# Kernel tuning notes

Hardware: AMD Instinct MI355X
Metric: run time of the kernel (lower is better)

The kernel has to match this reference:

```python
import jax, jax.numpy as jnp
import numpy as np

N_NODES = 100000
N_EDGES = 1600000
IN_F = 128
HID = 16
NEG_SLOPE = 0.2


def setup_inputs() -> dict:
    key = jax.random.key(0)
    ks = jax.random.split(key, 12)
    x = jax.random.normal(ks[0], (N_NODES, IN_F), dtype=jnp.float32)
    edge_index = jax.random.randint(ks[1], (2, N_EDGES), 0, N_NODES, dtype=jnp.int32)
    s1 = 1.0 / np.sqrt(IN_F)
    s2 = 1.0 / np.sqrt(2 * HID)
    # layer 1: heads=2, out=16, concat -> 32
    W1 = jax.random.normal(ks[2], (IN_F, 2 * HID), dtype=jnp.float32) * s1
    a_src1 = jax.random.normal(ks[3], (2, HID), dtype=jnp.float32) * s2
    a_dst1 = jax.random.normal(ks[4], (2, HID), dtype=jnp.float32) * s2
    b1 = jnp.zeros((2 * HID,), dtype=jnp.float32)
    # layer 2: heads=1, out=1
    W2 = jax.random.normal(ks[5], (2 * HID, 1), dtype=jnp.float32) * s2
    a_src2 = jax.random.normal(ks[6], (1, 1), dtype=jnp.float32)
    a_dst2 = jax.random.normal(ks[7], (1, 1), dtype=jnp.float32)
    b2 = jnp.zeros((1,), dtype=jnp.float32)
    return {"x": x, "edge_index": edge_index, "W1": W1, "a_src1": a_src1,
            "a_dst1": a_dst1, "b1": b1, "W2": W2, "a_src2": a_src2,
            "a_dst2": a_dst2, "b2": b2}


def gat_conv(x, src, dst, W, a_src, a_dst, bias, heads, out_ch, concat):
    # PyG GATConv: linear proj, per-edge leaky-relu score, segment softmax over
    # incoming edges (dst), scatter-add aggregation. Self loops already in src/dst.
    n = x.shape[0]
    h = (x @ W).reshape(n, heads, out_ch)                      # [N,H,C]
    alpha_s = (h * a_src[None]).sum(-1)                        # [N,H]
    alpha_d = (h * a_dst[None]).sum(-1)                        # [N,H]
    e = jax.nn.leaky_relu(alpha_s[src] + alpha_d[dst], NEG_SLOPE)  # [E,H]
    m = jax.lax.stop_gradient(jax.ops.segment_max(e, dst, num_segments=n))
    ex = jnp.exp(e - m[dst])
    denom = jax.ops.segment_sum(ex, dst, num_segments=n)       # [N,H]
    alpha = ex / (denom[dst] + 1e-16)                          # [E,H]
    out = jax.ops.segment_sum(alpha[..., None] * h[src], dst, num_segments=n)  # [N,H,C]
    out = out.reshape(n, heads * out_ch) if concat else out.mean(axis=1)
    return out + bias


def reference(x, edge_index, W1, a_src1, a_dst1, b1, W2, a_src2, a_dst2, b2):
    n = x.shape[0]
    loop = jnp.arange(n, dtype=edge_index.dtype)
    src = jnp.concatenate([edge_index[0], loop])
    dst = jnp.concatenate([edge_index[1], loop])
    h = jax.nn.elu(gat_conv(x, src, dst, W1, a_src1, a_dst1, b1, 2, HID, True))
    out = gat_conv(h, src, dst, W2, a_src2, a_dst2, b2, 1, 1, False)
    return out
```

## Files before the change

### kernel.cpp

```cpp
#include <hip/hip_runtime.h>
#include <math.h>

#define IN_F 128
#define C1 32
#define NEG 0.2f
#define BSZ 128
#define CAP 2560
#define EPB 16384
#define TPW 2

typedef _Float16 h16;
typedef _Float16 h16x2 __attribute__((ext_vector_type(2)));
typedef _Float16 h16x4 __attribute__((ext_vector_type(4)));
typedef _Float16 h16x8 __attribute__((ext_vector_type(8)));
typedef float f32x4 __attribute__((ext_vector_type(4)));

__device__ __forceinline__ float leaky(float x) { return x >= 0.f ? x : NEG * x; }

__global__ __launch_bounds__(256)
void k_fat(const float* __restrict__ x, const float* __restrict__ W1,
           const float* __restrict__ a_s, const float* __restrict__ a_d,
           h16* __restrict__ h1h, float* __restrict__ as1,
           float* __restrict__ ad1, int N,
           const int* __restrict__ ei, int E, int ET, int nbk,
           int* __restrict__ bcnt, int* __restrict__ ebuf, int nproj) {
    __shared__ int smem[2048];
    int t = threadIdx.x;
    if ((int)blockIdx.x < nproj) {
        int wid = t >> 6, lane = t & 63;
        int q = lane >> 4, r = lane & 15;
        h16x8 Bf[2][4];
        #pragma unroll
        for (int ct = 0; ct < 2; ++ct)
            #pragma unroll
            for (int kc = 0; kc < 4; ++kc)
                #pragma unroll
                for (int j = 0; j < 8; ++j)
                    Bf[ct][kc][j] = (h16)W1[(kc * 32 + q * 8 + j) * C1 + ct * 16 + r];
        float a_s0 = a_s[r], a_s1v = a_s[16 + r];
        float a_d0 = a_d[r], a_d1v = a_d[16 + r];
        #pragma unroll
        for (int tt = 0; tt < TPW; ++tt) {
            int tile = (blockIdx.x * 4 + wid) * TPW + tt;
            int m0 = tile << 4;
            if (m0 >= N) break;
            int row = m0 + r; if (row >= N) row = N - 1;
            const float* xr = x + (size_t)row * IN_F + q * 8;
            f32x4 acc0 = {0.f, 0.f, 0.f, 0.f};
            f32x4 acc1 = {0.f, 0.f, 0.f, 0.f};
            #pragma unroll
            for (int kc = 0; kc < 4; ++kc) {
                float4 xa = *(const float4*)(xr + kc * 32);
                float4 xb = *(const float4*)(xr + kc * 32 + 4);
                h16x8 A;
                A[0] = (h16)xa.x; A[1] = (h16)xa.y; A[2] = (h16)xa.z; A[3] = (h16)xa.w;
                A[4] = (h16)xb.x; A[5] = (h16)xb.y; A[6] = (h16)xb.z; A[7] = (h16)xb.w;
                acc0 = __builtin_amdgcn_mfma_f32_16x16x32_f16(A, Bf[0][kc], acc0, 0, 0, 0);
                acc1 = __builtin_amdgcn_mfma_f32_16x16x32_f16(A, Bf[1][kc], acc1, 0, 0, 0);
            }
            #pragma unroll
            for (int reg = 0; reg < 4; ++reg) {
                int node = m0 + q * 4 + reg;
                bool vld = node < N;
                float h0 = acc0[reg], h1 = acc1[reg];
                if (vld) {
                    h1h[(size_t)node * C1 + r]      = (h16)h0;
                    h1h[(size_t)node * C1 + 16 + r] = (h16)h1;
                }
                float s0 = h0 * a_s0, s1 = h1 * a_s1v;
                float d0 = h0 * a_d0, d1 = h1 * a_d1v;
                s0 += __shfl_xor(s0, 1); s0 += __shfl_xor(s0, 2); s0 += __shfl_xor(s0, 4); s0 += __shfl_xor(s0, 8);
                s1 += __shfl_xor(s1, 1); s1 += __shfl_xor(s1, 2); s1 += __shfl_xor(s1, 4); s1 += __shfl_xor(s1, 8);
                d0 += __shfl_xor(d0, 1); d0 += __shfl_xor(d0, 2); d0 += __shfl_xor(d0, 4); d0 += __shfl_xor(d0, 8);
                d1 += __shfl_xor(d1, 1); d1 += __shfl_xor(d1, 2); d1 += __shfl_xor(d1, 4); d1 += __shfl_xor(d1, 8);
                if (vld && r == 0) {
                    *(float2*)&as1[node * 2] = make_float2(s0, s1);
                    *(float2*)&ad1[node * 2] = make_float2(d0, d1);
                }
            }
        }
    } else {
        int* hist = smem;
        int* lcur = smem + 1024;
        int bid = blockIdx.x - nproj;
        hist[t] = 0; hist[t + 256] = 0; hist[t + 512] = 0; hist[t + 768] = 0;
        __syncthreads();
        int i0 = bid * EPB, i1 = min(ET, i0 + EPB);
        for (int i = i0 + t; i < i1; i += 256) {
            int d = (i < E) ? ei[E + i] : (i - E);
            atomicAdd(&hist[d >> 7], 1);
        }
        __syncthreads();
        for (int b = t; b < nbk; b += 256) {
            int h = hist[b];
            int base = h ? atomicAdd(&bcnt[b], h) : 0;
            lcur[b] = b * CAP + base;
        }
        __syncthreads();
        for (int i = i0 + t; i < i1; i += 256) {
            int s, d;
            if (i < E) { s = ei[i]; d = ei[E + i]; } else { s = d = i - E; }
            int bkt = d >> 7;
            int pos = atomicAdd(&lcur[bkt], 1);
            if (pos < (bkt + 1) * CAP)
                ebuf[pos] = (s << 7) | (d & 127);
        }
    }
}

__global__ __launch_bounds__(512)
void k_bagg(const int* __restrict__ bcnt, const int* __restrict__ ebuf,
            int N, int nbk, int ET,
            const float* __restrict__ as1, const float* __restrict__ ad1,
            const float* __restrict__ b1, const float* __restrict__ W2,
            const h16* __restrict__ h1h, int* __restrict__ off,
            int* __restrict__ csr1, float* __restrict__ p2) {
    __shared__ int2 elist[CAP];
    __shared__ int deg[BSZ], sst[BSZ], cur[BSZ];
    __shared__ float adl[BSZ * 2];
    __shared__ int red[8];
    int b = blockIdx.x, t = threadIdx.x;
    int cnt = min(bcnt[b], CAP);
    int ebase = b * CAP;
    int n0 = b * BSZ;
    int part = 0;
    for (int k = t; k < b; k += 512) part += min(bcnt[k], CAP);
    part += __shfl_xor(part, 1);  part += __shfl_xor(part, 2);
    part += __shfl_xor(part, 4);  part += __shfl_xor(part, 8);
    part += __shfl_xor(part, 16); part += __shfl_xor(part, 32);
    if ((t & 63) == 0) red[t >> 6] = part;
    if (t < BSZ) {
        deg[t] = 0;
        int n = n0 + t;
        float2 v = (n < N) ? ((const float2*)ad1)[n] : make_float2(0.f, 0.f);
        adl[t * 2] = v.x; adl[t * 2 + 1] = v.y;
    }
    __syncthreads();
    int fbase = red[0] + red[1] + red[2] + red[3] + red[4] + red[5] + red[6] + red[7];
    if (b == nbk - 1 && t == 0) off[N] = ET;
    for (int i = t; i < cnt; i += 512)
        atomicAdd(&deg[ebuf[ebase + i] & 127], 1);
    __syncthreads();
    int v = (t < BSZ) ? deg[t] : 0;
    __syncthreads();
    for (int o = 1; o < BSZ; o <<= 1) {
        int xv = (t >= o && t < BSZ) ? deg[t - o] : 0;
        __syncthreads();
        if (t < BSZ) deg[t] += xv;
        __syncthreads();
    }
    if (t < BSZ) {
        int excl = deg[t] - v;
        sst[t] = excl; cur[t] = excl;
        if (n0 + t < N) off[n0 + t] = fbase + excl;
    }
    __syncthreads();
    for (int i = t; i < cnt; i += 512) {
        int e = ebuf[ebase + i];
        int dl = e & 127, s = e >> 7;
        float2 asv = ((const float2*)as1)[s];
        float w0 = __expf(leaky(asv.x + adl[dl * 2 + 0]));
        float w1 = __expf(leaky(asv.y + adl[dl * 2 + 1]));
        h16x2 wp = { (h16)w0, (h16)w1 };
        int p = atomicAdd(&cur[dl], 1);
        int2 rec; rec.x = s; rec.y = *(int*)&wp;
        elist[p] = rec;
        csr1[fbase + p] = s;
    }
    __syncthreads();
    int l = t & 7, slot = t >> 3, c0 = l * 4, head = l >> 2;
    float b1l[4] = { b1[c0], b1[c0 + 1], b1[c0 + 2], b1[c0 + 3] };
    float w2l[4] = { W2[c0], W2[c0 + 1], W2[c0 + 2], W2[c0 + 3] };
    #pragma unroll
    for (int pass = 0; pass < 2; ++pass) {
        int dl = pass * 64 + slot;
        int node = n0 + dl;
        if (node >= N) break;
        int j0 = sst[dl], j1 = deg[dl];
        float den = 0.f, a0 = 0.f, a1 = 0.f, a2 = 0.f, a3 = 0.f;
        for (int j = j0; j < j1; j += 8) {
            #pragma unroll
            for (int k = 0; k < 8; ++k) {
                int jj = j + k;
                bool valid = jj < j1;
                jj = valid ? jj : j0;
                int2 e = elist[jj];
                int s = e.x;
                h16x2 wv = *(h16x2*)&e.y;
                float w = valid ? (float)(head ? wv.y : wv.x) : 0.f;
                h16x4 hv = *(const h16x4*)(h1h + ((size_t)s << 5) + c0);
                den += w;
                a0 = fmaf(w, (float)hv.x, a0);
                a1 = fmaf(w, (float)hv.y, a1);
                a2 = fmaf(w, (float)hv.z, a2);
                a3 = fmaf(w, (float)hv.w, a3);
            }
        }
        float inv = 1.f / (den + 1e-16f);
        float o, val = 0.f;
        o = a0 * inv + b1l[0]; o = o > 0.f ? o : expm1f(o); val = fmaf(o, w2l[0], val);
        o = a1 * inv + b1l[1]; o = o > 0.f ? o : expm1f(o); val = fmaf(o, w2l[1], val);
        o = a2 * inv + b1l[2]; o = o > 0.f ? o : expm1f(o); val = fmaf(o, w2l[2], val);
        o = a3 * inv + b1l[3]; o = o > 0.f ? o : expm1f(o); val = fmaf(o, w2l[3], val);
        val += __shfl_xor(val, 1); val += __shfl_xor(val, 2); val += __shfl_xor(val, 4);
        if (l == 0) p2[node] = val;
    }
}

__global__ __launch_bounds__(256)
void k_l2(const int* __restrict__ off, const int* __restrict__ csr1,
          const float* __restrict__ p2, const float* __restrict__ as2,
          const float* __restrict__ ad2, const float* __restrict__ b2,
          float* __restrict__ out, int N) {
    int tid = blockIdx.x * 256 + threadIdx.x;
    int g = tid >> 3, l = tid & 7;
    if (g >= N) return;
    float A = as2[0];
    float Bc = ad2[0] * p2[g];
    float den = 0.f, num = 0.f;
    int j0 = off[g], j1 = off[g + 1];
    for (int j = j0 + l; j < j1; j += 8) {
        float ps = p2[csr1[j]];
        float w = __expf(leaky(fmaf(ps, A, Bc)));
        den += w;
        num = fmaf(w, ps, num);
    }
    den += __shfl_xor(den, 1); den += __shfl_xor(den, 2); den += __shfl_xor(den, 4);
    num += __shfl_xor(num, 1); num += __shfl_xor(num, 2); num += __shfl_xor(num, 4);
    if (l == 0) out[g] = num / (den + 1e-16f) + b2[0];
}

extern "C" void kernel_launch(void* const* d_in, const int* in_sizes, int n_in,
                              void* d_out, int out_size, void* d_ws, size_t ws_size,
                              hipStream_t stream) {
    const float* x    = (const float*)d_in[0];
    const int*   ei   = (const int*)d_in[1];
    const float* W1   = (const float*)d_in[2];
    const float* a_s1 = (const float*)d_in[3];
    const float* a_d1 = (const float*)d_in[4];
    const float* b1   = (const float*)d_in[5];
    const float* W2   = (const float*)d_in[6];
    const float* a_s2 = (const float*)d_in[7];
    const float* a_d2 = (const float*)d_in[8];
    const float* b2   = (const float*)d_in[9];
    float* out = (float*)d_out;

    const int N  = in_sizes[0] / IN_F;
    const int E  = in_sizes[1] / 2;
    const int ET = E + N;
    const int nbk = (N + BSZ - 1) / BSZ;

    float* w   = (float*)d_ws;
    float* as1 = w; w += (size_t)2 * N;
    float* ad1 = w; w += (size_t)2 * N;
    float* p2  = w; w += (size_t)N;
    h16* h1h   = (h16*)w;
    w += (size_t)16 * N;
    int* iw     = (int*)w;
    int* bcnt   = iw; iw += 1024;
    int* off    = iw; iw += (N + 1);
    int* csr1   = iw; iw += ET;
    int* ebuf   = iw; iw += (size_t)nbk * CAP;

    const int B = 256;
    const int ntile = (N + 15) / 16;
    const int nproj = (ntile + 4 * TPW - 1) / (4 * TPW);
    const int nblkA = (ET + EPB - 1) / EPB;

    hipMemsetAsync(bcnt, 0, 1024 * sizeof(int), stream);
    k_fat <<<nproj + nblkA, B, 0, stream>>>(x, W1, a_s1, a_d1, h1h, as1, ad1, N,
                                            ei, E, ET, nbk, bcnt, ebuf, nproj);
    k_bagg<<<nbk, 512, 0, stream>>>(bcnt, ebuf, N, nbk, ET, as1, ad1, b1, W2,
                                    h1h, off, csr1, p2);
    k_l2  <<<(N * 8 + B - 1) / B, B, 0, stream>>>(off, csr1, p2, a_s2, a_d2, b2, out, N);
}
```

Before: 210.0 us.

## Split bucket aggregation into half-bucket blocks and cache edges in LDS during binning

The bucketed aggregation kernel now runs two blocks per 128-node bucket, each handling 64 destination nodes with a smaller LDS edge list. This doubles the block count and lowers LDS use per block, so more blocks can be resident. The cost is that each block re-reads the whole bucket's edges and recomputes the degree scan. The binning blocks now process smaller edge chunks (EPB 2048) and keep the loaded (src,dst) pairs in LDS, so the second pass no longer re-reads edge_index from global memory. Together this launches many more binning blocks, each issuing its own global atomics on bucket counters.

```diff
diff --git a/kernel.cpp b/kernel.cpp
--- a/kernel.cpp
+++ b/kernel.cpp
@@ -5,8 +5,10 @@
 #define C1 32
 #define NEG 0.2f
 #define BSZ 128
+#define HB 64
 #define CAP 2560
-#define EPB 16384
+#define CAPH 1536
+#define EPB 2048
 #define TPW 2
 
 typedef _Float16 h16;
@@ -24,7 +26,7 @@
            float* __restrict__ ad1, int N,
            const int* __restrict__ ei, int E, int ET, int nbk,
            int* __restrict__ bcnt, int* __restrict__ ebuf, int nproj) {
-    __shared__ int smem[2048];
+    __shared__ int smem[6144];
     int t = threadIdx.x;
     if ((int)blockIdx.x < nproj) {
         int wid = t >> 6, lane = t & 63;
@@ -82,12 +84,15 @@
     } else {
         int* hist = smem;
         int* lcur = smem + 1024;
+        int2* ecache = (int2*)(smem + 2048);
         int bid = blockIdx.x - nproj;
         hist[t] = 0; hist[t + 256] = 0; hist[t + 512] = 0; hist[t + 768] = 0;
         __syncthreads();
         int i0 = bid * EPB, i1 = min(ET, i0 + EPB);
         for (int i = i0 + t; i < i1; i += 256) {
-            int d = (i < E) ? ei[E + i] : (i - E);
+            int s, d;
+            if (i < E) { s = ei[i]; d = ei[E + i]; } else { s = d = i - E; }
+            ecache[i - i0] = make_int2(s, d);
             atomicAdd(&hist[d >> 7], 1);
         }
         __syncthreads();
@@ -98,12 +103,11 @@
         }
         __syncthreads();
         for (int i = i0 + t; i < i1; i += 256) {
-            int s, d;
-            if (i < E) { s = ei[i]; d = ei[E + i]; } else { s = d = i - E; }
-            int bkt = d >> 7;
+            int2 e = ecache[i - i0];
+            int bkt = e.y >> 7;
             int pos = atomicAdd(&lcur[bkt], 1);
             if (pos < (bkt + 1) * CAP)
-                ebuf[pos] = (s << 7) | (d & 127);
+                ebuf[pos] = (e.x << 7) | (e.y & 127);
         }
     }
 }
@@ -115,29 +119,30 @@
             const float* __restrict__ b1, const float* __restrict__ W2,
             const h16* __restrict__ h1h, int* __restrict__ off,
             int* __restrict__ csr1, float* __restrict__ p2) {
-    __shared__ int2 elist[CAP];
-    __shared__ int deg[BSZ], sst[BSZ], cur[BSZ];
-    __shared__ float adl[BSZ * 2];
+    __shared__ int2 elist[CAPH];
+    __shared__ int deg[BSZ], sst[BSZ], cur[HB];
+    __shared__ float adl[HB * 2];
     __shared__ int red[8];
-    int b = blockIdx.x, t = threadIdx.x;
+    int blk = blockIdx.x, t = threadIdx.x;
+    int b = blk >> 1, h = blk & 1;
     int cnt = min(bcnt[b], CAP);
     int ebase = b * CAP;
-    int n0 = b * BSZ;
+    int n0 = b * BSZ + h * HB;
     int part = 0;
     for (int k = t; k < b; k += 512) part += min(bcnt[k], CAP);
     part += __shfl_xor(part, 1);  part += __shfl_xor(part, 2);
     part += __shfl_xor(part, 4);  part += __shfl_xor(part, 8);
     part += __shfl_xor(part, 16); part += __shfl_xor(part, 32);
     if ((t & 63) == 0) red[t >> 6] = part;
-    if (t < BSZ) {
-        deg[t] = 0;
+    if (t < BSZ) deg[t] = 0;
+    if (t < HB) {
         int n = n0 + t;
         float2 v = (n < N) ? ((const float2*)ad1)[n] : make_float2(0.f, 0.f);
         adl[t * 2] = v.x; adl[t * 2 + 1] = v.y;
     }
     __syncthreads();
     int fbase = red[0] + red[1] + red[2] + red[3] + red[4] + red[5] + red[6] + red[7];
-    if (b == nbk - 1 && t == 0) off[N] = ET;
+    if (blk == 2 * nbk - 1 && t == 0) off[N] = ET;
     for (int i = t; i < cnt; i += 512)
         atomicAdd(&deg[ebuf[ebase + i] & 127], 1);
     __syncthreads();
@@ -149,62 +154,68 @@
         if (t < BSZ) deg[t] += xv;
         __syncthreads();
     }
-    if (t < BSZ) {
-        int excl = deg[t] - v;
-        sst[t] = excl; cur[t] = excl;
-        if (n0 + t < N) off[n0 + t] = fbase + excl;
+    if (t < BSZ) sst[t] = deg[t] - v;
+    __syncthreads();
+    int hbase = h ? deg[HB - 1] : 0;
+    if (t < HB) {
+        int dl = h * HB + t;
+        cur[t] = sst[dl] - hbase;
+        int node = n0 + t;
+        if (node < N) off[node] = fbase + sst[dl];
     }
     __syncthreads();
     for (int i = t; i < cnt; i += 512) {
         int e = ebuf[ebase + i];
-        int dl = e & 127, s = e >> 7;
+        int dl = e & 127;
+        if ((dl >> 6) != h) continue;
+        int dll = dl & (HB - 1), s = e >> 7;
         float2 asv = ((const float2*)as1)[s];
-        float w0 = __expf(leaky(asv.x + adl[dl * 2 + 0]));
-        float w1 = __expf(leaky(asv.y + adl[dl * 2 + 1]));
+        float w0 = __expf(leaky(asv.x + adl[dll * 2 + 0]));
+        float w1 = __expf(leaky(asv.y + adl[dll * 2 + 1]));
         h16x2 wp = { (h16)w0, (h16)w1 };
-        int p = atomicAdd(&cur[dl], 1);
-        int2 rec; rec.x = s; rec.y = *(int*)&wp;
-        elist[p] = rec;
-        csr1[fbase + p] = s;
+        int p = atomicAdd(&cur[dll], 1);
+        if (p < CAPH) {
+            int2 rec; rec.x = s; rec.y = *(int*)&wp;
+            elist[p] = rec;
+            csr1[fbase + hbase + p] = s;
+        }
     }
     __syncthreads();
     int l = t & 7, slot = t >> 3, c0 = l * 4, head = l >> 2;
+    int node = n0 + slot;
+    if (node >= N) return;
+    int dl = h * HB + slot;
+    int j0 = min(sst[dl] - hbase, CAPH);
+    int j1 = min(deg[dl] - hbase, CAPH);
     float b1l[4] = { b1[c0], b1[c0 + 1], b1[c0 + 2], b1[c0 + 3] };
     float w2l[4] = { W2[c0], W2[c0 + 1], W2[c0 + 2], W2[c0 + 3] };
-    #pragma unroll
-    for (int pass = 0; pass < 2; ++pass) {
-        int dl = pass * 64 + slot;
-        int node = n0 + dl;
-        if (node >= N) break;
-        int j0 = sst[dl], j1 = deg[dl];
-        float den = 0.f, a0 = 0.f, a1 = 0.f, a2 = 0.f, a3 = 0.f;
-        for (int j = j0; j < j1; j += 8) {
-            #pragma unroll
-            for (int k = 0; k < 8; ++k) {
-                int jj = j + k;
-                bool valid = jj < j1;
-                jj = valid ? jj : j0;
-                int2 e = elist[jj];
-                int s = e.x;
-                h16x2 wv = *(h16x2*)&e.y;
-                float w = valid ? (float)(head ? wv.y : wv.x) : 0.f;
-                h16x4 hv = *(const h16x4*)(h1h + ((size_t)s << 5) + c0);
-                den += w;
-                a0 = fmaf(w, (float)hv.x, a0);
-                a1 = fmaf(w, (float)hv.y, a1);
-                a2 = fmaf(w, (float)hv.z, a2);
-                a3 = fmaf(w, (float)hv.w, a3);
-            }
-        }
-        float inv = 1.f / (den + 1e-16f);
-        float o, val = 0.f;
-        o = a0 * inv + b1l[0]; o = o > 0.f ? o : expm1f(o); val = fmaf(o, w2l[0], val);
-        o = a1 * inv + b1l[1]; o = o > 0.f ? o : expm1f(o); val = fmaf(o, w2l[1], val);
-        o = a2 * inv + b1l[2]; o = o > 0.f ? o : expm1f(o); val = fmaf(o, w2l[2], val);
-        o = a3 * inv + b1l[3]; o = o > 0.f ? o : expm1f(o); val = fmaf(o, w2l[3], val);
-        val += __shfl_xor(val, 1); val += __shfl_xor(val, 2); val += __shfl_xor(val, 4);
-        if (l == 0) p2[node] = val;
-    }
+    float den = 0.f, a0 = 0.f, a1 = 0.f, a2 = 0.f, a3 = 0.f;
+    for (int j = j0; j < j1; j += 8) {
+        #pragma unroll
+        for (int k = 0; k < 8; ++k) {
+            int jj = j + k;
+            bool valid = jj < j1;
+            jj = valid ? jj : j0;
+            int2 e = elist[jj];
+            int s = e.x;
+            h16x2 wv = *(h16x2*)&e.y;
+            float w = valid ? (float)(head ? wv.y : wv.x) : 0.f;
+            h16x4 hv = *(const h16x4*)(h1h + ((size_t)s << 5) + c0);
+            den += w;
+            a0 = fmaf(w, (float)hv.x, a0);
+            a1 = fmaf(w, (float)hv.y, a1);
+            a2 = fmaf(w, (float)hv.z, a2);
+            a3 = fmaf(w, (float)hv.w, a3);
+        }
+    }
+    float inv = 1.f / (den + 1e-16f);
+    float o, val = 0.f;
+    o = a0 * inv + b1l[0]; o = o > 0.f ? o : expm1f(o); val = fmaf(o, w2l[0], val);
+    o = a1 * inv + b1l[1]; o = o > 0.f ? o : expm1f(o); val = fmaf(o, w2l[1], val);
+    o = a2 * inv + b1l[2]; o = o > 0.f ? o : expm1f(o); val = fmaf(o, w2l[2], val);
+    o = a3 * inv + b1l[3]; o = o > 0.f ? o : expm1f(o); val = fmaf(o, w2l[3], val);
+    val += __shfl_xor(val, 1); val += __shfl_xor(val, 2); val += __shfl_xor(val, 4);
+    if (l == 0) p2[node] = val;
 }
 
 __global__ __launch_bounds__(256)
@@ -270,7 +281,7 @@
     hipMemsetAsync(bcnt, 0, 1024 * sizeof(int), stream);
     k_fat <<<nproj + nblkA, B, 0, stream>>>(x, W1, a_s1, a_d1, h1h, as1, ad1, N,
                                             ei, E, ET, nbk, bcnt, ebuf, nproj);
-    k_bagg<<<nbk, 512, 0, stream>>>(bcnt, ebuf, N, nbk, ET, as1, ad1, b1, W2,
-                                    h1h, off, csr1, p2);
+    k_bagg<<<nbk * 2, 512, 0, stream>>>(bcnt, ebuf, N, nbk, ET, as1, ad1, b1, W2,
+                                        h1h, off, csr1, p2);
     k_l2  <<<(N * 8 + B - 1) / B, B, 0, stream>>>(off, csr1, p2, a_s2, a_d2, b2, out, N);
 }
```

Measured after the change: 186.3 us. -11.3%, faster.

## Halve destination bucket size, cache edges in LDS, widen per-lane aggregation

Applied to the files above, without the earlier changes.

Destination buckets shrink from 128 to 64 nodes, so there are about twice as many aggregation blocks, each with 256 threads and a smaller LDS edge list. Blocks that partition edges now cover 2048 edges and keep them in LDS between the histogram and scatter passes, so the edge indices are read from global memory once. The degree prefix sum becomes a single-wavefront shuffle scan instead of a barrier loop. Each node is now handled by 4 lanes that load 8 halves per neighbour row instead of 8 lanes loading 4. The trade-offs are more buckets and more global atomics on bcnt, and a bucket can overflow its 1312-edge capacity if the degree distribution is skewed.

```diff
diff --git a/kernel.cpp b/kernel.cpp
--- a/kernel.cpp
+++ b/kernel.cpp
@@ -4,10 +4,11 @@
 #define IN_F 128
 #define C1 32
 #define NEG 0.2f
-#define BSZ 128
-#define CAP 2560
-#define EPB 16384
+#define BSZ 64
+#define CAPB 1312
+#define EPB 2048
 #define TPW 2
+#define HISTN 1664
 
 typedef _Float16 h16;
 typedef _Float16 h16x2 __attribute__((ext_vector_type(2)));
@@ -24,7 +25,7 @@
            float* __restrict__ ad1, int N,
            const int* __restrict__ ei, int E, int ET, int nbk,
            int* __restrict__ bcnt, int* __restrict__ ebuf, int nproj) {
-    __shared__ int smem[2048];
+    __shared__ int smem[2 * HISTN + 4096];
     int t = threadIdx.x;
     if ((int)blockIdx.x < nproj) {
         int wid = t >> 6, lane = t & 63;
@@ -81,50 +82,53 @@
         }
     } else {
         int* hist = smem;
-        int* lcur = smem + 1024;
+        int* lcur = smem + HISTN;
+        int2* ecache = (int2*)(smem + 2 * HISTN);
         int bid = blockIdx.x - nproj;
-        hist[t] = 0; hist[t + 256] = 0; hist[t + 512] = 0; hist[t + 768] = 0;
+        for (int b = t; b < nbk; b += 256) hist[b] = 0;
         __syncthreads();
         int i0 = bid * EPB, i1 = min(ET, i0 + EPB);
         for (int i = i0 + t; i < i1; i += 256) {
-            int d = (i < E) ? ei[E + i] : (i - E);
-            atomicAdd(&hist[d >> 7], 1);
+            int s, d;
+            if (i < E) { s = ei[i]; d = ei[E + i]; } else { s = d = i - E; }
+            ecache[i - i0] = make_int2(s, d);
+            atomicAdd(&hist[d >> 6], 1);
         }
         __syncthreads();
         for (int b = t; b < nbk; b += 256) {
             int h = hist[b];
             int base = h ? atomicAdd(&bcnt[b], h) : 0;
-            lcur[b] = b * CAP + base;
+            lcur[b] = b * CAPB + base;
         }
         __syncthreads();
         for (int i = i0 + t; i < i1; i += 256) {
-            int s, d;
-            if (i < E) { s = ei[i]; d = ei[E + i]; } else { s = d = i - E; }
-            int bkt = d >> 7;
+            int2 e = ecache[i - i0];
+            int bkt = e.y >> 6;
             int pos = atomicAdd(&lcur[bkt], 1);
-            if (pos < (bkt + 1) * CAP)
-                ebuf[pos] = (s << 7) | (d & 127);
-        }
-    }
-}
-
-__global__ __launch_bounds__(512)
+            if (pos < (bkt + 1) * CAPB)
+                ebuf[pos] = (e.x << 6) | (e.y & 63);
+        }
+    }
+}
+
+__global__ __launch_bounds__(256)
 void k_bagg(const int* __restrict__ bcnt, const int* __restrict__ ebuf,
             int N, int nbk, int ET,
             const float* __restrict__ as1, const float* __restrict__ ad1,
             const float* __restrict__ b1, const float* __restrict__ W2,
             const h16* __restrict__ h1h, int* __restrict__ off,
             int* __restrict__ csr1, float* __restrict__ p2) {
-    __shared__ int2 elist[CAP];
+    __shared__ int2 elist[CAPB];
     __shared__ int deg[BSZ], sst[BSZ], cur[BSZ];
     __shared__ float adl[BSZ * 2];
-    __shared__ int red[8];
+    __shared__ float b1s[C1], w2s[C1];
+    __shared__ int red[4];
     int b = blockIdx.x, t = threadIdx.x;
-    int cnt = min(bcnt[b], CAP);
-    int ebase = b * CAP;
     int n0 = b * BSZ;
+    int cnt = min(bcnt[b], CAPB);
+    int ebase = b * CAPB;
     int part = 0;
-    for (int k = t; k < b; k += 512) part += min(bcnt[k], CAP);
+    for (int k = t; k < b; k += 256) part += min(bcnt[k], CAPB);
     part += __shfl_xor(part, 1);  part += __shfl_xor(part, 2);
     part += __shfl_xor(part, 4);  part += __shfl_xor(part, 8);
     part += __shfl_xor(part, 16); part += __shfl_xor(part, 32);
@@ -135,29 +139,29 @@
         float2 v = (n < N) ? ((const float2*)ad1)[n] : make_float2(0.f, 0.f);
         adl[t * 2] = v.x; adl[t * 2 + 1] = v.y;
     }
-    __syncthreads();
-    int fbase = red[0] + red[1] + red[2] + red[3] + red[4] + red[5] + red[6] + red[7];
+    if (t >= 64 && t < 64 + C1) { b1s[t - 64] = b1[t - 64]; w2s[t - 64] = W2[t - 64]; }
     if (b == nbk - 1 && t == 0) off[N] = ET;
-    for (int i = t; i < cnt; i += 512)
-        atomicAdd(&deg[ebuf[ebase + i] & 127], 1);
-    __syncthreads();
-    int v = (t < BSZ) ? deg[t] : 0;
-    __syncthreads();
-    for (int o = 1; o < BSZ; o <<= 1) {
-        int xv = (t >= o && t < BSZ) ? deg[t - o] : 0;
-        __syncthreads();
-        if (t < BSZ) deg[t] += xv;
-        __syncthreads();
-    }
-    if (t < BSZ) {
-        int excl = deg[t] - v;
-        sst[t] = excl; cur[t] = excl;
-        if (n0 + t < N) off[n0 + t] = fbase + excl;
-    }
-    __syncthreads();
-    for (int i = t; i < cnt; i += 512) {
+    __syncthreads();
+    int fbase = red[0] + red[1] + red[2] + red[3];
+    for (int i = t; i < cnt; i += 256)
+        atomicAdd(&deg[ebuf[ebase + i] & 63], 1);
+    __syncthreads();
+    if (t < 64) {
+        int orig = deg[t], v = orig;
+        #pragma unroll
+        for (int o = 1; o < 64; o <<= 1) {
+            int u = __shfl_up(v, o);
+            if (t >= o) v += u;
+        }
+        deg[t] = v;
+        int e = v - orig;
+        sst[t] = e; cur[t] = e;
+        if (n0 + t < N) off[n0 + t] = fbase + e;
+    }
+    __syncthreads();
+    for (int i = t; i < cnt; i += 256) {
         int e = ebuf[ebase + i];
-        int dl = e & 127, s = e >> 7;
+        int dl = e & 63, s = e >> 6;
         float2 asv = ((const float2*)as1)[s];
         float w0 = __expf(leaky(asv.x + adl[dl * 2 + 0]));
         float w1 = __expf(leaky(asv.y + adl[dl * 2 + 1]));
@@ -168,43 +172,39 @@
         csr1[fbase + p] = s;
     }
     __syncthreads();
-    int l = t & 7, slot = t >> 3, c0 = l * 4, head = l >> 2;
-    float b1l[4] = { b1[c0], b1[c0 + 1], b1[c0 + 2], b1[c0 + 3] };
-    float w2l[4] = { W2[c0], W2[c0 + 1], W2[c0 + 2], W2[c0 + 3] };
+    int l = t & 3, slot = t >> 2, c0 = l * 8, head = l >> 1;
+    int node = n0 + slot;
+    if (node >= N) return;
+    int j0 = sst[slot], j1 = deg[slot];
+    float den = 0.f;
+    float acc[8] = {0.f, 0.f, 0.f, 0.f, 0.f, 0.f, 0.f, 0.f};
+    for (int j = j0; j < j1; j += 8) {
+        #pragma unroll
+        for (int k = 0; k < 8; ++k) {
+            int jj = j + k;
+            bool valid = jj < j1;
+            jj = valid ? jj : j0;
+            int2 e = elist[jj];
+            int s = e.x;
+            h16x2 wv = *(h16x2*)&e.y;
+            float w = valid ? (float)(head ? wv.y : wv.x) : 0.f;
+            h16x8 hv = *(const h16x8*)(h1h + ((size_t)s << 5) + c0);
+            den += w;
+            #pragma unroll
+            for (int i2 = 0; i2 < 8; ++i2)
+                acc[i2] = fmaf(w, (float)hv[i2], acc[i2]);
+        }
+    }
+    float inv = 1.f / (den + 1e-16f);
+    float val = 0.f;
     #pragma unroll
-    for (int pass = 0; pass < 2; ++pass) {
-        int dl = pass * 64 + slot;
-        int node = n0 + dl;
-        if (node >= N) break;
-        int j0 = sst[dl], j1 = deg[dl];
-        float den = 0.f, a0 = 0.f, a1 = 0.f, a2 = 0.f, a3 = 0.f;
-        for (int j = j0; j < j1; j += 8) {
-            #pragma unroll
-            for (int k = 0; k < 8; ++k) {
-                int jj = j + k;
-                bool valid = jj < j1;
-                jj = valid ? jj : j0;
-                int2 e = elist[jj];
-                int s = e.x;
-                h16x2 wv = *(h16x2*)&e.y;
-                float w = valid ? (float)(head ? wv.y : wv.x) : 0.f;
-                h16x4 hv = *(const h16x4*)(h1h + ((size_t)s << 5) + c0);
-                den += w;
-                a0 = fmaf(w, (float)hv.x, a0);
-                a1 = fmaf(w, (float)hv.y, a1);
-                a2 = fmaf(w, (float)hv.z, a2);
-                a3 = fmaf(w, (float)hv.w, a3);
-            }
-        }
-        float inv = 1.f / (den + 1e-16f);
-        float o, val = 0.f;
-        o = a0 * inv + b1l[0]; o = o > 0.f ? o : expm1f(o); val = fmaf(o, w2l[0], val);
-        o = a1 * inv + b1l[1]; o = o > 0.f ? o : expm1f(o); val = fmaf(o, w2l[1], val);
-        o = a2 * inv + b1l[2]; o = o > 0.f ? o : expm1f(o); val = fmaf(o, w2l[2], val);
-        o = a3 * inv + b1l[3]; o = o > 0.f ? o : expm1f(o); val = fmaf(o, w2l[3], val);
-        val += __shfl_xor(val, 1); val += __shfl_xor(val, 2); val += __shfl_xor(val, 4);
-        if (l == 0) p2[node] = val;
-    }
+    for (int i2 = 0; i2 < 8; ++i2) {
+        float o = acc[i2] * inv + b1s[c0 + i2];
+        o = o > 0.f ? o : expm1f(o);
+        val = fmaf(o, w2s[c0 + i2], val);
+    }
+    val += __shfl_xor(val, 1); val += __shfl_xor(val, 2);
+    if (l == 0) p2[node] = val;
 }
 
 __global__ __launch_bounds__(256)
@@ -257,20 +257,20 @@
     h16* h1h   = (h16*)w;
     w += (size_t)16 * N;
     int* iw     = (int*)w;
-    int* bcnt   = iw; iw += 1024;
+    int* bcnt   = iw; iw += 2048;
     int* off    = iw; iw += (N + 1);
     int* csr1   = iw; iw += ET;
-    int* ebuf   = iw; iw += (size_t)nbk * CAP;
+    int* ebuf   = iw; iw += (size_t)nbk * CAPB;
 
     const int B = 256;
     const int ntile = (N + 15) / 16;
     const int nproj = (ntile + 4 * TPW - 1) / (4 * TPW);
     const int nblkA = (ET + EPB - 1) / EPB;
 
-    hipMemsetAsync(bcnt, 0, 1024 * sizeof(int), stream);
+    hipMemsetAsync(bcnt, 0, 2048 * sizeof(int), stream);
     k_fat <<<nproj + nblkA, B, 0, stream>>>(x, W1, a_s1, a_d1, h1h, as1, ad1, N,
                                             ei, E, ET, nbk, bcnt, ebuf, nproj);
-    k_bagg<<<nbk, 512, 0, stream>>>(bcnt, ebuf, N, nbk, ET, as1, ad1, b1, W2,
-                                    h1h, off, csr1, p2);
+    k_bagg<<<nbk, B, 0, stream>>>(bcnt, ebuf, N, nbk, ET, as1, ad1, b1, W2,
+                                  h1h, off, csr1, p2);
     k_l2  <<<(N * 8 + B - 1) / B, B, 0, stream>>>(off, csr1, p2, a_s2, a_d2, b2, out, N);
 }
```

Result: faster. 182.7 us (-13.0%).
